# Kernel optimization log

Measured on AMD Instinct MI355X. Metric: run time of the kernel, lower is better.

Reference implementation:

```python
import jax, jax.numpy as jnp
import numpy as np

C, PH, PW, H, W = 10, 7, 7, 34, 34
STRIDE = 8.0
S = 4  # sample_per_part


def setup_inputs() -> dict:
    key = jax.random.key(0)
    k1, k2, k3, k4, k5 = jax.random.split(key, 5)
    N = 30000
    ft = jax.random.normal(k1, (1, C * PH * PW, H, W), dtype=jnp.float32)
    x1 = jax.random.uniform(k2, (N,), dtype=jnp.float32) * 200.0
    y1 = jax.random.uniform(k3, (N,), dtype=jnp.float32) * 200.0
    bw = jax.random.uniform(k4, (N,), dtype=jnp.float32) * 70.0 + 2.0
    bh = jax.random.uniform(k5, (N,), dtype=jnp.float32) * 70.0 + 2.0
    rois = jnp.stack([jnp.zeros((N,), jnp.float32), x1, y1, x1 + bw, y1 + bh], axis=1)
    return {"ft_add_left_right": ft, "rois": rois}


def reference(ft_add_left_right, rois):
    ft = ft_add_left_right[0].reshape(C, PH, PW, H, W)
    roi_start_w = rois[:, 1] / STRIDE
    roi_start_h = rois[:, 2] / STRIDE
    roi_end_w = rois[:, 3] / STRIDE
    roi_end_h = rois[:, 4] / STRIDE
    # torch.threshold(x, 0.1, 0.1): x if x > 0.1 else 0.1
    roi_height = jnp.where(roi_end_h - roi_start_h > 0.1, roi_end_h - roi_start_h, 0.1)
    roi_width = jnp.where(roi_end_w - roi_start_w > 0.1, roi_end_w - roi_start_w, 0.1)
    bin_size_h = roi_height / PH
    bin_size_w = roi_width / PW
    sub_h = bin_size_h / S
    sub_w = bin_size_w / S

    gh, gw = jnp.meshgrid(jnp.arange(PH), jnp.arange(PW), indexing='ij')
    phs = gh.reshape(-1, 1)  # [49,1]
    pws = gw.reshape(-1, 1)  # [49,1]
    hstart = jnp.floor(roi_start_h + phs * bin_size_h)  # [49,N]
    wstart = jnp.floor(roi_start_w + pws * bin_size_w)  # [49,N]

    N = rois.shape[0]
    sum_ = jnp.zeros((C, PH * PW, N), jnp.float32)
    count = jnp.zeros((PH * PW, N), jnp.float32)

    for ih in range(S):
        for iw in range(S):
            w = wstart + (iw + 0.5) * sub_w  # [49,N]
            h = hstart + (ih + 0.5) * sub_h
            keep = (w > -1) & (w < W) & (h > -1) & (h < H)
            x1 = jnp.floor(w).astype(jnp.int32)
            x2 = jnp.ceil(w).astype(jnp.int32)
            y1 = jnp.floor(h).astype(jnp.int32)
            y2 = jnp.ceil(h).astype(jnp.int32)
            x1v = (x1 >= 0) & (x1 < W)
            x2v = (x2 >= 0) & (x2 < W)
            y1v = (y1 >= 0) & (y1 < H)
            y2v = (y2 >= 0) & (y2 < H)
            x1 = jnp.clip(x1, 0, W - 1)
            x2 = jnp.clip(x2, 0, W - 1)
            y1 = jnp.clip(y1, 0, H - 1)
            y2 = jnp.clip(y2, 0, H - 1)
            dist_x = w - x1
            dist_y = h - y1
            # gathers: result [C,49,N]
            v11 = ft[:, phs, pws, y1, x1]
            v12 = ft[:, phs, pws, y2, x1]
            v21 = ft[:, phs, pws, y1, x2]
            v22 = ft[:, phs, pws, y2, x2]
            # faithful to source: ALL four masks zero value11 only (source bug)
            bad11 = (~x1v & y1v) | (~x1v & y2v) | (~x2v & y1v) | (~x2v & y2v)
            v11 = jnp.where(bad11, 0.0, v11)
            value = ((1 - dist_x) * (1 - dist_y) * v11
                     + (1 - dist_x) * dist_y * v12
                     + dist_x * (1 - dist_y) * v21
                     + dist_x * dist_y * v22)
            sum_ = sum_ + jnp.where(keep, value, 0.0)
            count = count + keep.astype(jnp.float32)

    out = jnp.where(count > 0, sum_ / jnp.maximum(count, 1.0), sum_)
    return jnp.transpose(out, (2, 0, 1))  # [N, C, 49]
```

## Files before the change

### kernel.cpp

```cpp
#include <hip/hip_runtime.h>
#include <hip/hip_fp16.h>


#define NC 10
#define NBIN 49
#define FH 34
#define FW 34
#define PLANE (FH * FW)
#define NPIX (NBIN * PLANE)
#define GPC 18882
#define RPB 16
#define TSTRIDE 491
#define NSIDE 14
#define NXCD 8
#define PREP_BLOCKS 56
#define KBUCKET 16384

__device__ __forceinline__ unsigned int roi_key(const float* __restrict__ rois, int n)
{
    const float rsw = rois[n * 5 + 1] * 0.125f;
    const float rsh = rois[n * 5 + 2] * 0.125f;
    const float rew = rois[n * 5 + 3] * 0.125f;
    const float reh = rois[n * 5 + 4] * 0.125f;
    float rh = reh - rsh; if (!(rh > 0.1f)) rh = 0.1f;
    float rw = rew - rsw; if (!(rw > 0.1f)) rw = 0.1f;
    const int y0 = min(31, max(0, (int)floorf(rsh)));
    const int x0 = min(31, max(0, (int)floorf(rsw)));
    const int bh = min(3, (int)(rh * (4.0f / 9.0f)));
    const int bw = min(3, (int)(rw * (4.0f / 9.0f)));
    return (unsigned int)(((((y0 << 5) | x0) << 2 | bh) << 2) | bw);
}

__global__ __launch_bounds__(1024) void zero_kernel(unsigned int* __restrict__ cursor)
{
    cursor[blockIdx.x * 1024 + threadIdx.x] = 0u;
}

__global__ __launch_bounds__(1024) void prep_hist_kernel(
    const float* __restrict__ ft, unsigned int* __restrict__ ftR,
    const float* __restrict__ rois, unsigned int* __restrict__ keys,
    unsigned int* __restrict__ cursor, int N)
{
    if (blockIdx.x >= PREP_BLOCKS) {
        const int n = (blockIdx.x - PREP_BLOCKS) * 1024 + threadIdx.x;
        if (n < N) {
            const unsigned int k = roi_key(rois, n);
            keys[n] = k;
            atomicAdd(&cursor[k], 1u);
        }
        return;
    }

    const int p = blockIdx.x * 1024 + threadIdx.x;
    if (p >= NPIX + 2) return;
    unsigned int h2[5];
    if (p < NPIX) {
#pragma unroll
        for (int c = 0; c < 5; ++c) {
            const __half lo = __float2half_rn(ft[(2 * c)     * NPIX + p]);
            const __half hi = __float2half_rn(ft[(2 * c + 1) * NPIX + p]);
            const __half2 hh = __halves2half2(lo, hi);
            h2[c] = *(const unsigned int*)&hh;
        }
    } else {
#pragma unroll
        for (int c = 0; c < 5; ++c) h2[c] = 0u;
    }
#pragma unroll
    for (int m = 0; m < 3; ++m) {
        if (p >= m) {
            const int t = p - m;
            const int g = t / 3;
            const int j = t - 3 * g;
            if (g < GPC) {
                unsigned int* d = ftR + ((size_t)m * GPC + g) * 16 + j * 5;
#pragma unroll
                for (int c = 0; c < 5; ++c) d[c] = h2[c];
            }
        }
    }
}

__global__ __launch_bounds__(1024) void scan_kernel(unsigned int* __restrict__ cursor)
{
    __shared__ unsigned int part[1024];
    const int t = threadIdx.x;
    unsigned int c[16];
    unsigned int s = 0;
#pragma unroll
    for (int i = 0; i < 16; ++i) { c[i] = cursor[t * 16 + i]; s += c[i]; }
    part[t] = s;
    __syncthreads();
    for (int off = 1; off < 1024; off <<= 1) {
        const unsigned int v = (t >= off) ? part[t - off] : 0u;
        __syncthreads();
        part[t] += v;
        __syncthreads();
    }
    unsigned int base = (t == 0) ? 0u : part[t - 1];
#pragma unroll
    for (int i = 0; i < 16; ++i) { cursor[t * 16 + i] = base; base += c[i]; }
}

__global__ __launch_bounds__(1024) void scatter_kernel(
    const unsigned int* __restrict__ keys, unsigned int* __restrict__ cursor,
    int* __restrict__ perm, int N)
{
    const int n = blockIdx.x * 1024 + threadIdx.x;
    if (n >= N) return;
    const unsigned int pos = atomicAdd(&cursor[keys[n]], 1u);
    perm[pos] = n;
}

__device__ __forceinline__ void fma2(float w, unsigned int u, float& s0, float& s1)
{
    const __half2 h = *(const __half2*)&u;
    s0 = fmaf(w, __half2float(__low2half(h)),  s0);
    s1 = fmaf(w, __half2float(__high2half(h)), s1);
}

__global__ __launch_bounds__(256, 4) void main_kernel(
    const float* __restrict__ rois, const unsigned int* __restrict__ ftR,
    const int* __restrict__ perm, const float* __restrict__ ft,
    float* __restrict__ out, int N, int use_t)
{
    __shared__ float sides[NSIDE][RPB][8];
    __shared__ float tile[RPB][TSTRIDE];

    const int nwg = gridDim.x;
    const int q = nwg / NXCD, rr = nwg % NXCD;
    const int xcd = blockIdx.x % NXCD, idx = blockIdx.x / NXCD;
    const int bid = (xcd < rr ? xcd * (q + 1) : rr * (q + 1) + (xcd - rr) * q) + idx;

    const int r = threadIdx.x & (RPB - 1);
    const int s = threadIdx.x >> 4;
    const int n = bid * RPB + r;
    const bool valid = (n < N);
    const int nn = (use_t && valid) ? perm[n] : n;

    float rsw = 0.f, rsh = 0.f, rew = 0.f, reh = 0.f;
    if (valid) {
        rsw = rois[nn * 5 + 1] * 0.125f;
        rsh = rois[nn * 5 + 2] * 0.125f;
        rew = rois[nn * 5 + 3] * 0.125f;
        reh = rois[nn * 5 + 4] * 0.125f;
    }
    float rheight = __fsub_rn(reh, rsh);
    if (!(rheight > 0.1f)) rheight = 0.1f;
    float rwidth = __fsub_rn(rew, rsw);
    if (!(rwidth > 0.1f)) rwidth = 0.1f;
    const float bsh   = __fdiv_rn(rheight, 7.0f);
    const float bsw   = __fdiv_rn(rwidth, 7.0f);
    const float sub_h = __fdiv_rn(bsh, 4.0f);
    const float sub_w = __fdiv_rn(bsw, 4.0f);

    if (s < NSIDE) {
        const bool isY = (s < 7);
        const int  k   = isY ? s : s - 7;
        const float st = isY ? rsh : rsw;
        const float bs = isY ? bsh : bsw;
        const float sb = isY ? sub_h : sub_w;
        const float start = floorf(__fadd_rn(st, __fmul_rn((float)k, bs)));

        float A[3] = {0.f, 0.f, 0.f}, B[3] = {0.f, 0.f, 0.f};
        float cnt = 0.f;
        int P0 = 0;
#pragma unroll
        for (int i = 0; i < 4; ++i) {
            const float h = __fadd_rn(start, __fmul_rn((float)i + 0.5f, sb));
            const bool ok = (h > -1.0f) && (h < 34.0f);
            const int p1 = (int)floorf(h);
            const int p2 = (int)ceilf(h);
            const bool v1 = (p1 >= 0) && (p1 < 34);
            const bool v2 = (p2 >= 0) && (p2 < 34);
            const int p1c = min(max(p1, 0), 33);
            const int p2c = min(max(p2, 0), 33);
            const float d = __fsub_rn(h, (float)p1c);
            if (i == 0) P0 = p1c;
            const int i1 = p1c - P0, i2 = p2c - P0;
            const float t1 = ok ? (1.0f - d) : 0.0f;
            const float t2 = ok ? d : 0.0f;
            const bool bsel = isY ? (v1 || v2) : ((!v1) || (!v2));
            const float tb = (ok && bsel) ? (1.0f - d) : 0.0f;
            cnt += ok ? 1.0f : 0.0f;
#pragma unroll
            for (int p = 0; p < 3; ++p) {
                A[p] += (i1 == p) ? t1 : 0.0f;
                A[p] += (i2 == p) ? t2 : 0.0f;
                B[p] += (i1 == p) ? tb : 0.0f;
            }
        }
        float* sp = &sides[s][r][0];
        sp[0] = A[0]; sp[1] = A[1]; sp[2] = A[2];
        sp[3] = B[0]; sp[4] = B[1]; sp[5] = B[2];
        sp[6] = cnt;  sp[7] = (float)P0;
    }
    __syncthreads();

#pragma unroll
    for (int j = 0; j < 4; ++j) {
        const int bin = j * RPB + s;
        if (valid && bin < NBIN) {
            const int ph = bin / 7;
            const int pw = bin - ph * 7;

            const float4 ya = *(const float4*)&sides[ph][r][0];
            const float4 yb = *(const float4*)&sides[ph][r][4];
            const float4 xa = *(const float4*)&sides[7 + pw][r][0];
            const float4 xb = *(const float4*)&sides[7 + pw][r][4];
            const float AY[3] = {ya.x, ya.y, ya.z};
            const float BY[3] = {ya.w, yb.x, yb.y};
            const float cntY  = yb.z;
            const int   Y0    = (int)yb.w;
            const float AX[3] = {xa.x, xa.y, xa.z};
            const float BX[3] = {xa.w, xb.x, xb.y};
            const float cntX  = xb.z;
            const int   X0    = (int)xb.w;

            const int binbase = bin * PLANE;
            const int rowo[3] = {binbase + Y0 * FW,
                                 binbase + min(Y0 + 1, FH - 1) * FW,
                                 binbase + min(Y0 + 2, FH - 1) * FW};

            float wgt[9];
#pragma unroll
            for (int p = 0; p < 3; ++p)
#pragma unroll
                for (int q2 = 0; q2 < 3; ++q2)
                    wgt[3 * p + q2] = AY[p] * AX[q2] - BY[p] * BX[q2];

            float sum[NC];
#pragma unroll
            for (int c = 0; c < NC; ++c) sum[c] = 0.f;

            if (use_t) {
                const int e = (FW - 1) - X0;
                unsigned int rv[3][15];
                float ew[3][3];
#pragma unroll
                for (int p = 0; p < 3; ++p) {
                    const float w0 = wgt[3 * p], w1 = wgt[3 * p + 1], w2 = wgt[3 * p + 2];
                    const float s12 = w1 + w2;
                    ew[p][0] = (e < 1) ? (w0 + s12) : w0;
                    ew[p][1] = (e < 1) ? 0.f : ((e < 2) ? s12 : w1);
                    ew[p][2] = (e < 2) ? 0.f : w2;
                    const bool rnz = (w0 != 0.0f) || (w1 != 0.0f) || (w2 != 0.0f);
                    const int fp = rnz ? (rowo[p] + X0) : binbase;
                    const int g = fp / 3;
                    const int m = fp - 3 * g;
                    const unsigned int* lp = ftR + ((size_t)m * GPC + g) * 16;
                    const uint4 a = *(const uint4*)lp;
                    const uint4 b = *(const uint4*)(lp + 4);
                    const uint4 c4 = *(const uint4*)(lp + 8);
                    const uint4 d4 = *(const uint4*)(lp + 12);
                    rv[p][0]  = a.x;  rv[p][1]  = a.y;  rv[p][2]  = a.z;  rv[p][3]  = a.w;
                    rv[p][4]  = b.x;  rv[p][5]  = b.y;  rv[p][6]  = b.z;  rv[p][7]  = b.w;
                    rv[p][8]  = c4.x; rv[p][9]  = c4.y; rv[p][10] = c4.z; rv[p][11] = c4.w;
                    rv[p][12] = d4.x; rv[p][13] = d4.y; rv[p][14] = d4.z;
                }
#pragma unroll
                for (int p = 0; p < 3; ++p)
#pragma unroll
                    for (int c = 0; c < 5; ++c) {
                        fma2(ew[p][0], rv[p][c],      sum[2 * c], sum[2 * c + 1]);
                        fma2(ew[p][1], rv[p][5 + c],  sum[2 * c], sum[2 * c + 1]);
                        fma2(ew[p][2], rv[p][10 + c], sum[2 * c], sum[2 * c + 1]);
                    }
            } else {
                const int colo[3] = {X0, min(X0 + 1, FW - 1), min(X0 + 2, FW - 1)};
                int off[9];
#pragma unroll
                for (int p = 0; p < 3; ++p)
#pragma unroll
                    for (int q2 = 0; q2 < 3; ++q2)
                        off[3 * p + q2] = (wgt[3 * p + q2] != 0.0f) ? (rowo[p] + colo[q2])
                                                                    : binbase;
#pragma unroll
                for (int k = 0; k < 9; ++k) {
                    const float w = wgt[k];
#pragma unroll
                    for (int c = 0; c < NC; ++c)
                        sum[c] = fmaf(w, ft[c * NPIX + off[k]], sum[c]);
                }
            }

            const float cnt = cntY * cntX;
            const float inv = (cnt > 0.0f) ? __fdiv_rn(1.0f, cnt) : 1.0f;
            float* tp = &tile[r][0];
#pragma unroll
            for (int c = 0; c < NC; ++c) tp[c * NBIN + bin] = sum[c] * inv;
        }
    }

    __syncthreads();

    const int n0 = bid * RPB;
    for (int i = threadIdx.x; i < RPB * (NC * NBIN); i += 256) {
        const int row = i / (NC * NBIN);
        const int col = i - row * (NC * NBIN);
        const int n2 = n0 + row;
        if (n2 < N) {
            const int nd = use_t ? perm[n2] : n2;
            out[(size_t)nd * (NC * NBIN) + col] = tile[row][col];
        }
    }
}

extern "C" void kernel_launch(void* const* d_in, const int* in_sizes, int n_in,
                              void* d_out, int out_size, void* d_ws, size_t ws_size,
                              hipStream_t stream) {
    const float* ft   = (const float*)d_in[0];
    const float* rois = (const float*)d_in[1];
    float* out        = (float*)d_out;
    const int N = in_sizes[1] / 5;

    const size_t ftr_bytes = (size_t)3 * GPC * 64;
    const size_t need = ftr_bytes + (size_t)KBUCKET * 4 + (size_t)8 * N;
    const int use_t = (ws_size >= need) ? 1 : 0;
    unsigned int* ftR    = (unsigned int*)d_ws;
    unsigned int* cursor = (unsigned int*)((char*)d_ws + ftr_bytes);
    unsigned int* keys   = cursor + KBUCKET;
    int*          perm   = (int*)(keys + N);

    if (use_t) {
        const int hb = (N + 1023) / 1024;
        zero_kernel<<<KBUCKET / 1024, 1024, 0, stream>>>(cursor);
        prep_hist_kernel<<<PREP_BLOCKS + hb, 1024, 0, stream>>>(ft, ftR, rois, keys, cursor, N);
        scan_kernel<<<1, 1024, 0, stream>>>(cursor);
        scatter_kernel<<<hb, 1024, 0, stream>>>(keys, cursor, perm, N);
    }
    main_kernel<<<(N + RPB - 1) / RPB, 256, 0, stream>>>(rois, ftR, perm, ft, out, N, use_t);
}
```

Before: 122.1 us.

## Fuse presort pipeline into one cooperative kernel with grid syncs

Replaces the four preprocessing launches (zero, pack/histogram, scan, scatter) with a single cooperative kernel of 64 blocks that separates the phases with grid-wide syncs. The aim is to cut the launch and inter-kernel gap overhead of the short preprocessing stages. In exchange, only 64 blocks do the feature packing and the ROI work, the single-block scan leaves the rest of the grid idle, and grid.sync adds its own cost. The old multi-kernel path stays as a fallback if the cooperative launch fails, and bounds clamps are added to perm indexing.

```diff
diff --git a/kernel.cpp b/kernel.cpp
--- a/kernel.cpp
+++ b/kernel.cpp
@@ -1,5 +1,8 @@
 #include <hip/hip_runtime.h>
 #include <hip/hip_fp16.h>
+#include <hip/hip_cooperative_groups.h>
+
+namespace cg = cooperative_groups;
 
 
 #define NC 10
@@ -15,6 +18,7 @@
 #define NXCD 8
 #define PREP_BLOCKS 56
 #define KBUCKET 16384
+#define COOP_BLOCKS 64
 
 __device__ __forceinline__ unsigned int roi_key(const float* __restrict__ rois, int n)
 {
@@ -31,28 +35,9 @@
     return (unsigned int)(((((y0 << 5) | x0) << 2 | bh) << 2) | bw);
 }
 
-__global__ __launch_bounds__(1024) void zero_kernel(unsigned int* __restrict__ cursor)
-{
-    cursor[blockIdx.x * 1024 + threadIdx.x] = 0u;
-}
-
-__global__ __launch_bounds__(1024) void prep_hist_kernel(
-    const float* __restrict__ ft, unsigned int* __restrict__ ftR,
-    const float* __restrict__ rois, unsigned int* __restrict__ keys,
-    unsigned int* __restrict__ cursor, int N)
-{
-    if (blockIdx.x >= PREP_BLOCKS) {
-        const int n = (blockIdx.x - PREP_BLOCKS) * 1024 + threadIdx.x;
-        if (n < N) {
-            const unsigned int k = roi_key(rois, n);
-            keys[n] = k;
-            atomicAdd(&cursor[k], 1u);
-        }
-        return;
-    }
-
-    const int p = blockIdx.x * 1024 + threadIdx.x;
-    if (p >= NPIX + 2) return;
+__device__ __forceinline__ void pack_pixel(
+    const float* __restrict__ ft, unsigned int* __restrict__ ftR, int p)
+{
     unsigned int h2[5];
     if (p < NPIX) {
 #pragma unroll
@@ -79,6 +64,76 @@
             }
         }
     }
+}
+
+__global__ __launch_bounds__(1024) void presort_kernel(
+    const float* __restrict__ ft, unsigned int* __restrict__ ftR,
+    const float* __restrict__ rois, unsigned int* __restrict__ keys,
+    unsigned int* __restrict__ cursor, int* __restrict__ perm, int N)
+{
+    __shared__ unsigned int part[1024];
+    cg::grid_group grid = cg::this_grid();
+    const int tid = blockIdx.x * 1024 + threadIdx.x;
+    const int nthr = COOP_BLOCKS * 1024;
+
+    for (int i = tid; i < KBUCKET; i += nthr) cursor[i] = 0u;
+    for (int p = tid; p < NPIX + 2; p += nthr) pack_pixel(ft, ftR, p);
+    grid.sync();
+
+    for (int n = tid; n < N; n += nthr) {
+        const unsigned int k = roi_key(rois, n);
+        keys[n] = k;
+        atomicAdd(&cursor[k], 1u);
+    }
+    grid.sync();
+
+    if (blockIdx.x == 0) {
+        const int t = threadIdx.x;
+        unsigned int c[16];
+        unsigned int s = 0;
+#pragma unroll
+        for (int i = 0; i < 16; ++i) { c[i] = cursor[t * 16 + i]; s += c[i]; }
+        part[t] = s;
+        __syncthreads();
+        for (int off = 1; off < 1024; off <<= 1) {
+            const unsigned int v = (t >= off) ? part[t - off] : 0u;
+            __syncthreads();
+            part[t] += v;
+            __syncthreads();
+        }
+        unsigned int base = (t == 0) ? 0u : part[t - 1];
+#pragma unroll
+        for (int i = 0; i < 16; ++i) { cursor[t * 16 + i] = base; base += c[i]; }
+    }
+    grid.sync();
+
+    for (int n = tid; n < N; n += nthr) {
+        const unsigned int pos = atomicAdd(&cursor[keys[n]], 1u);
+        if (pos < (unsigned int)N) perm[pos] = n;
+    }
+}
+
+__global__ __launch_bounds__(1024) void zero_kernel(unsigned int* __restrict__ cursor)
+{
+    cursor[blockIdx.x * 1024 + threadIdx.x] = 0u;
+}
+
+__global__ __launch_bounds__(1024) void prep_hist_kernel(
+    const float* __restrict__ ft, unsigned int* __restrict__ ftR,
+    const float* __restrict__ rois, unsigned int* __restrict__ keys,
+    unsigned int* __restrict__ cursor, int N)
+{
+    if (blockIdx.x >= PREP_BLOCKS) {
+        const int n = (blockIdx.x - PREP_BLOCKS) * 1024 + threadIdx.x;
+        if (n < N) {
+            const unsigned int k = roi_key(rois, n);
+            keys[n] = k;
+            atomicAdd(&cursor[k], 1u);
+        }
+        return;
+    }
+    const int p = blockIdx.x * 1024 + threadIdx.x;
+    if (p < NPIX + 2) pack_pixel(ft, ftR, p);
 }
 
 __global__ __launch_bounds__(1024) void scan_kernel(unsigned int* __restrict__ cursor)
@@ -109,7 +164,7 @@
     const int n = blockIdx.x * 1024 + threadIdx.x;
     if (n >= N) return;
     const unsigned int pos = atomicAdd(&cursor[keys[n]], 1u);
-    perm[pos] = n;
+    if (pos < (unsigned int)N) perm[pos] = n;
 }
 
 __device__ __forceinline__ void fma2(float w, unsigned int u, float& s0, float& s1)
@@ -136,7 +191,7 @@
     const int s = threadIdx.x >> 4;
     const int n = bid * RPB + r;
     const bool valid = (n < N);
-    const int nn = (use_t && valid) ? perm[n] : n;
+    const int nn = (use_t && valid) ? min(max(perm[n], 0), N - 1) : n;
 
     float rsw = 0.f, rsh = 0.f, rew = 0.f, reh = 0.f;
     if (valid) {
@@ -300,7 +355,7 @@
         const int col = i - row * (NC * NBIN);
         const int n2 = n0 + row;
         if (n2 < N) {
-            const int nd = use_t ? perm[n2] : n2;
+            const int nd = use_t ? min(max(perm[n2], 0), N - 1) : n2;
             out[(size_t)nd * (NC * NBIN) + col] = tile[row][col];
         }
     }
@@ -323,11 +378,20 @@
     int*          perm   = (int*)(keys + N);
 
     if (use_t) {
-        const int hb = (N + 1023) / 1024;
-        zero_kernel<<<KBUCKET / 1024, 1024, 0, stream>>>(cursor);
-        prep_hist_kernel<<<PREP_BLOCKS + hb, 1024, 0, stream>>>(ft, ftR, rois, keys, cursor, N);
-        scan_kernel<<<1, 1024, 0, stream>>>(cursor);
-        scatter_kernel<<<hb, 1024, 0, stream>>>(keys, cursor, perm, N);
+        int Nv = N;
+        void* args[] = {(void*)&ft, (void*)&ftR, (void*)&rois, (void*)&keys,
+                        (void*)&cursor, (void*)&perm, (void*)&Nv};
+        hipError_t err = hipLaunchCooperativeKernel(
+            (const void*)presort_kernel, dim3(COOP_BLOCKS), dim3(1024),
+            args, 0, stream);
+        if (err != hipSuccess) {
+            const int hb = (N + 1023) / 1024;
+            zero_kernel<<<KBUCKET / 1024, 1024, 0, stream>>>(cursor);
+            prep_hist_kernel<<<PREP_BLOCKS + hb, 1024, 0, stream>>>(
+                ft, ftR, rois, keys, cursor, N);
+            scan_kernel<<<1, 1024, 0, stream>>>(cursor);
+            scatter_kernel<<<hb, 1024, 0, stream>>>(keys, cursor, perm, N);
+        }
     }
     main_kernel<<<(N + RPB - 1) / RPB, 256, 0, stream>>>(rois, ftR, perm, ft, out, N, use_t);
 }
```

Measured after the change: 166.3 us. +36.2%, slower.
